# Kernel optimization log

Measured on AMD Instinct MI355X. Metric: run time of the kernel, lower is better.

Reference implementation:

```python
import jax, jax.numpy as jnp
import numpy as np

B, N, K, D, V, L = 16, 512, 16, 256, 64, 2


def setup_inputs() -> dict:
    key = jax.random.key(0)
    ks = jax.random.split(key, 20)
    inp = {
        "node_reps": jax.random.normal(ks[0], (B, N, D), dtype=jnp.float32),
        "mask": jax.random.uniform(ks[1], (B, N), dtype=jnp.float32),
        "in_indices": jax.random.randint(ks[2], (B, N, K), 0, N),
        "in_edges": jax.random.randint(ks[3], (B, N, K), 0, V),
        "in_mask": jax.random.uniform(ks[4], (B, N, K), dtype=jnp.float32),
        "out_indices": jax.random.randint(ks[5], (B, N, K), 0, N),
        "out_edges": jax.random.randint(ks[6], (B, N, K), 0, V),
        "out_mask": jax.random.uniform(ks[7], (B, N, K), dtype=jnp.float32),
        "edge_emb": jax.random.normal(ks[8], (V, D), dtype=jnp.float32) * 0.02,
        # packed gate weights, order [ig, fg, og, cell] along last dim
        "Wi": jax.random.normal(ks[9], (2 * D, 4 * D), dtype=jnp.float32) * 0.02,
        "Wo": jax.random.normal(ks[10], (2 * D, 4 * D), dtype=jnp.float32) * 0.02,
        "Ui": jax.random.normal(ks[11], (2 * D, 4 * D), dtype=jnp.float32) * 0.02,
        "Uo": jax.random.normal(ks[12], (2 * D, 4 * D), dtype=jnp.float32) * 0.02,
        "bi": jnp.zeros((4 * D,), dtype=jnp.float32),
        "bo": jnp.zeros((4 * D,), dtype=jnp.float32),
        "bui": jnp.zeros((4 * D,), dtype=jnp.float32),
        "buo": jnp.zeros((4 * D,), dtype=jnp.float32),
    }
    return inp


def _agg(h, idx, edge_reps, nmask):
    # gather neighbor states: [B,N,K,D]
    neigh = h[jnp.arange(h.shape[0])[:, None, None], idx]
    x = jnp.concatenate([neigh, edge_reps], axis=-1) * nmask[..., None]
    return x.sum(axis=2)  # [B,N,2D]


def reference(node_reps, mask, in_indices, in_edges, in_mask,
              out_indices, out_edges, out_mask,
              edge_emb, Wi, Wo, Ui, Uo, bi, bo, bui, buo):
    in_edge_reps = edge_emb[in_edges]    # [B,N,K,D]
    out_edge_reps = edge_emb[out_edges]  # [B,N,K,D]

    in_reps = _agg(node_reps, in_indices, in_edge_reps, in_mask)     # [B,N,2D]
    out_reps = _agg(node_reps, out_indices, out_edge_reps, out_mask)  # [B,N,2D]
    z_static = in_reps @ Wi + bi + out_reps @ Wo + bo  # [B,N,4D]

    h = node_reps
    c = jnp.zeros_like(node_reps)
    reps = []
    for _ in range(L):
        in_pre = _agg(h, in_indices, in_edge_reps, in_mask)
        out_pre = _agg(h, out_indices, out_edge_reps, out_mask)
        z = z_static + in_pre @ Ui + bui + out_pre @ Uo + buo  # [B,N,4D]
        ig, fg, og, ci = jnp.split(z, 4, axis=-1)
        ig = jax.nn.sigmoid(ig)
        fg = jax.nn.sigmoid(fg)
        og = jax.nn.sigmoid(og)
        ci = jnp.tanh(ci)
        c_new = fg * c + ig * ci
        h_new = og * jnp.tanh(c_new)
        c = c_new * mask[..., None]
        h = h_new * mask[..., None]
        reps.append(h)
    return (jnp.stack(reps, axis=0), h, c)
```

## Files before the change

### kernel.cpp

```cpp
#include <hip/hip_runtime.h>
#include <math.h>

#define Kn 16
#define Dd 256
#define NC 1024
#define MR 8192

typedef _Float16 h8 __attribute__((ext_vector_type(8)));
typedef _Float16 h4 __attribute__((ext_vector_type(4)));
typedef _Float16 h2 __attribute__((ext_vector_type(2)));
typedef float f4 __attribute__((ext_vector_type(4)));

__device__ __forceinline__ void gload16(_Float16* lds, const _Float16* g) {
  __builtin_amdgcn_global_load_lds(
      (const __attribute__((address_space(1))) void*)g,
      (__attribute__((address_space(3))) void*)lds, 16, 0, 0);
}

__device__ __forceinline__ float fsigm(float x) { return 1.f / (1.f + __expf(-x)); }
__device__ __forceinline__ float ftanh(float x) { return 2.f / (1.f + __expf(-2.f * x)) - 1.f; }

__global__ __launch_bounds__(256) void prep_kernel(
    const float* __restrict__ node_reps, const float* __restrict__ emb,
    const int* __restrict__ iidx, const float* __restrict__ im,
    const int* __restrict__ oidx, const float* __restrict__ om,
    const int* __restrict__ ie, const int* __restrict__ oe,
    const float* __restrict__ Wi, const float* __restrict__ Wo,
    const float* __restrict__ Ui, const float* __restrict__ Uo,
    const float* __restrict__ bi, const float* __restrict__ bo,
    const float* __restrict__ bui, const float* __restrict__ buo,
    _Float16* __restrict__ X, _Float16* __restrict__ W0f,
    _Float16* __restrict__ Wlf, float* __restrict__ biasq,
    _Float16* __restrict__ n16) {
  __shared__ __align__(16) char smem[40960];
  const int b = blockIdx.x, t = threadIdx.x;

  if (b < 64) {
    float* seT = (float*)smem;
    float* sa = (float*)(smem + 8192);
    const int vgrp = b >> 2, cq = b & 3;
    const int dir = vgrp >> 3;
    const int v0 = (vgrp & 7) * 8;
    const float* Wa = dir ? Wo : Wi;
    const float* Ua = dir ? Uo : Ui;
#pragma unroll
    for (int r = 0; r < 8; r++) seT[t * 8 + r] = emb[(v0 + r) * 256 + t];
    __syncthreads();

    const int l = t & 63, ds = t >> 6;
    const int cp0 = cq * 256 + l * 4;
    const int g = (cp0 >> 4) & 3;
    const int d0 = ((cp0 >> 6) << 4) + (cp0 & 15);
    const int c0 = g * 256 + d0;
    const float* wp = Wa + (size_t)(256 + ds * 64) * NC + c0;
    const float* up = Ua + (size_t)(256 + ds * 64) * NC + c0;
    const float* sT = seT + (ds * 64) * 8;

    f4 av[8] = {};
    for (int bb8 = 0; bb8 < 8; bb8++) {
      f4 wv8[8], uv8[8];
#pragma unroll
      for (int ii = 0; ii < 8; ii++) {
        const int dd = bb8 * 8 + ii;
        wv8[ii] = *(const f4*)(wp + (size_t)dd * NC);
        uv8[ii] = *(const f4*)(up + (size_t)dd * NC);
      }
      __builtin_amdgcn_sched_barrier(0);
#pragma unroll
      for (int ii = 0; ii < 8; ii++) {
        const int dd = bb8 * 8 + ii;
        const f4 wv = wv8[ii] + uv8[ii];
        const f4 s0 = *(const f4*)&sT[dd * 8];
        const f4 s1 = *(const f4*)&sT[dd * 8 + 4];
        av[0] += s0[0] * wv; av[1] += s0[1] * wv;
        av[2] += s0[2] * wv; av[3] += s0[3] * wv;
        av[4] += s1[0] * wv; av[5] += s1[1] * wv;
        av[6] += s1[2] * wv; av[7] += s1[3] * wv;
      }
    }
#pragma unroll
    for (int r = 0; r < 8; r++) *(f4*)&sa[((ds * 8 + r) * 64 + l) * 4] = av[r];
    __syncthreads();
#pragma unroll
    for (int it = 0; it < 2; it++) {
      const int item = t + it * 256;
      const int r = item >> 6, fl = item & 63;
      f4 s = {0.f, 0.f, 0.f, 0.f};
#pragma unroll
      for (int d = 0; d < 4; d++) s += *(const f4*)&sa[((d * 8 + r) * 64 + fl) * 4];
      const int vvg = vgrp * 8 + r;
      const int kt = 16 + (vvg >> 5);
      const int lhi = (vvg >> 3) & 3;
      const int j = vvg & 7;
      const int cpb = cq * 256 + fl * 4;
#pragma unroll
      for (int i = 0; i < 4; i++) {
        const int cp = cpb + i;
        W0f[kt * 32768 + (cp >> 4) * 512 + (lhi * 16 + (cp & 15)) * 8 + j] = (_Float16)s[i];
      }
    }
  } else if (b < 96) {
    const int p = b - 64;
    const int kk = t >> 3;
    const int tc = t & 7;
    const int k = (p & 15) * 32 + kk;
    const float* rowp;
    const float* rowp2 = nullptr;
    if (p < 16) {
      rowp  = (k < 256) ? Wi + (size_t)k * NC : Wo + (size_t)(k - 256) * NC;
      rowp2 = (k < 256) ? Ui + (size_t)k * NC : Uo + (size_t)(k - 256) * NC;
    } else {
      rowp  = (k < 256) ? Ui + (size_t)k * NC : Uo + (size_t)(k - 256) * NC;
    }
    _Float16* dst = (p < 16) ? (W0f + p * 32768) : (Wlf + (p - 16) * 32768);
    const int lane0 = (kk >> 3) * 16;
    const int j = kk & 7;
    for (int bb8 = 0; bb8 < 4; bb8++) {
      f4 w8[8], u8[8];
#pragma unroll
      for (int ii = 0; ii < 8; ii++) {
        const int c = (bb8 * 8 + ii) * 32 + tc * 4;
        w8[ii] = *(const f4*)(rowp + c);
        if (p < 16) u8[ii] = *(const f4*)(rowp2 + c);
      }
      __builtin_amdgcn_sched_barrier(0);
#pragma unroll
      for (int ii = 0; ii < 8; ii++) {
        const int c = (bb8 * 8 + ii) * 32 + tc * 4;
        const int g = c >> 8, d = c & 255;
        const int nt = 4 * (d >> 4) + g;
        const int lb = lane0 + (d & 15);
        f4 v = w8[ii];
        if (p < 16) v += u8[ii];
#pragma unroll
        for (int q = 0; q < 4; q++)
          dst[nt * 512 + (lb + q) * 8 + j] = (_Float16)v[q];
      }
    }
  } else if (b < 224) {
    const int cb = b - 96;
#pragma unroll
    for (int r = 0; r < 8; r++) {
      const int off = cb * 16384 + r * 2048 + t * 8;
      const f4 v0 = *(const f4*)(node_reps + off);
      const f4 v1 = *(const f4*)(node_reps + off + 4);
      h8 o;
#pragma unroll
      for (int jj = 0; jj < 4; jj++) { o[jj] = (_Float16)v0[jj]; o[jj + 4] = (_Float16)v1[jj]; }
      *(h8*)&n16[off] = o;
    }
  } else if (b < 736) {
    const int lane = t & 63;
    const int wid = t >> 6;
    const int half = lane >> 5;
    const int sel = lane >> 4, p16 = lane & 15;
    const int vmine = 2 * lane - half * 64;
#pragma unroll
    for (int j = 0; j < 4; j++) {
      const int row = (b - 224) * 16 + wid * 4 + j;
      const int bb = row * Kn + p16;
      const int* ap = (sel == 0)   ? (iidx + bb)
                      : (sel == 1) ? ((const int*)im + bb)
                      : (sel == 2) ? (oidx + bb)
                                   : ((const int*)om + bb);
      const int cmb = *ap;
      const int cmbe = *(((lane & 16) ? oe : ie) + bb);
      float b0 = 0.f, b1 = 0.f;
#pragma unroll
      for (int k = 0; k < 16; k++) {
        const int ec = __shfl(cmbe, (half << 4) | k, 64);
        const float mc = __int_as_float(__shfl(cmb, (lane & 32) | 16 | k, 64));
        b0 += (ec == vmine) ? mc : 0.f;
        b1 += (ec == vmine + 1) ? mc : 0.f;
      }
      h2 bp;
      bp[0] = (_Float16)b0;
      bp[1] = (_Float16)b1;
      *(h2*)&X[(size_t)row * NC + 512 + lane * 2] = bp;
    }
  } else {
#pragma unroll
    for (int i = 0; i < 4; i++) {
      const int cq = t * 4 + i;
      const int dd = cq >> 2, g = cq & 3;
      const int c = g * 256 + dd;
      biasq[cq] = bi[c] + bo[c] + bui[c] + buo[c];
    }
  }
}

__global__ __launch_bounds__(256, 4) void agg_kernel(
    const _Float16* __restrict__ src,
    const int* __restrict__ iidx, const float* __restrict__ im,
    const int* __restrict__ oidx, const float* __restrict__ om,
    _Float16* __restrict__ X) {
  const int lane = threadIdx.x & 63;
  const int wid = threadIdx.x >> 6;
  const int b = blockIdx.x;
  const int row = (b & 7) * 1024 + (b >> 3) * 4 + wid;
  const int half = lane >> 5;
  const int lc = lane & 31;
  const int sel = lane >> 4, p16 = lane & 15;

  const int bb = row * Kn + p16;
  const int* ap = (sel == 0)   ? (iidx + bb)
                  : (sel == 1) ? ((const int*)im + bb)
                  : (sel == 2) ? (oidx + bb)
                               : ((const int*)om + bb);
  const int cmb = *ap;

  const int hb = row & ~511;
  const _Float16* hp = src + ((size_t)hb << 8) + (lc << 3);

  h8 w[16];
#pragma unroll
  for (int k = 0; k < 16; k++) {
    const int ik = __shfl(cmb, (lane & 32) | k, 64);
    w[k] = *(const h8*)(hp + ((size_t)ik << 8));
  }
  __builtin_amdgcn_sched_barrier(0);

  float acc[8] = {};
#pragma unroll
  for (int k = 0; k < 16; k++) {
    const float mk = __int_as_float(__shfl(cmb, (lane & 32) | 16 | k, 64));
#pragma unroll
    for (int c = 0; c < 8; c++) acc[c] += mk * (float)w[k][c];
  }

  h8 o;
#pragma unroll
  for (int c = 0; c < 8; c++) o[c] = (_Float16)acc[c];
  *(h8*)&X[(size_t)row * NC + half * 256 + lc * 8] = o;
}

template <bool WITH_Z>
__global__ __launch_bounds__(256) void fused_gemm(
    const _Float16* __restrict__ A, const _Float16* __restrict__ Wf,
    const float* __restrict__ biasq, _Float16* __restrict__ zq,
    const float* __restrict__ mask, const float* __restrict__ node_reps,
    float* __restrict__ reps, float* __restrict__ hbuf,
    _Float16* __restrict__ d16, float* __restrict__ cbuf) {
  constexpr int KT = WITH_Z ? 20 : 16;
  constexpr int D = 4;
  __shared__ __align__(16) _Float16 lds[3][8192];

  const int wg = (blockIdx.x & 7) * 64 + (blockIdx.x >> 3);
  const int bm = wg >> 3, bn = wg & 7;
  const int tid = threadIdx.x, lane = tid & 63, wid = tid >> 6;
  const int wr = wid >> 1, wc = wid & 1;
  const int lr = lane & 15, lg = lane >> 4;

  f4 acc[4][4] = {};

  const _Float16* srcA0 = A + (size_t)(bm * 128 + 2 * wid * 16 + lr) * NC + lg * 8;
  const _Float16* srcB0 = Wf + ((size_t)bn * 8 + 2 * wid) * 512 + lane * 8;
  const int woff = 2 * wid * 512;

  auto stage = [&](int buf, int kt) {
    _Float16* base = lds[buf];
    const _Float16* sa = srcA0 + kt * 32;
    gload16(base + woff, sa);
    gload16(base + woff + 512, sa + 16 * NC);
    const _Float16* sb = srcB0 + (size_t)kt * 32768;
    gload16(base + 4096 + woff, sb);
    gload16(base + 4096 + woff + 512, sb + 512);
  };

  stage(0, 0);
  stage(1, 1);
  asm volatile("s_waitcnt vmcnt(%0)" :: "i"(D) : "memory");
  __builtin_amdgcn_s_barrier();

  int cur = 0;
  for (int kt = 0; kt < KT; kt++) {
    if (kt + 2 < KT) stage(cur == 0 ? 2 : cur - 1, kt + 2);

    const _Float16* base = lds[cur];
    h8 a[4], bfr[4];
#pragma unroll
    for (int m = 0; m < 4; m++) a[m] = *(const h8*)&base[(wr * 4 + m) * 512 + lane * 8];
#pragma unroll
    for (int n = 0; n < 4; n++) bfr[n] = *(const h8*)&base[4096 + (wc * 4 + n) * 512 + lane * 8];
    asm volatile("s_waitcnt lgkmcnt(0)" ::: "memory");
    __builtin_amdgcn_sched_barrier(0);

    __builtin_amdgcn_s_setprio(1);
#pragma unroll
    for (int m = 0; m < 4; m++)
#pragma unroll
      for (int n = 0; n < 4; n++)
        acc[m][n] = __builtin_amdgcn_mfma_f32_16x16x32_f16(a[m], bfr[n], acc[m][n], 0, 0, 0);
    __builtin_amdgcn_s_setprio(0);

    if (kt + 2 < KT) asm volatile("s_waitcnt vmcnt(%0)" :: "i"(D) : "memory");
    else             asm volatile("s_waitcnt vmcnt(0)" ::: "memory");
    __builtin_amdgcn_sched_barrier(0);
    __builtin_amdgcn_s_barrier();

    cur = (cur == 2) ? 0 : cur + 1;
  }

  const int d = (bn * 2 + wc) * 16 + lr;
  const int row0 = bm * 128 + wr * 64;
  f4 bq = {0.f, 0.f, 0.f, 0.f};
  if (WITH_Z) bq = *(const f4*)&biasq[d * 4];
#pragma unroll
  for (int i = 0; i < 4; i++) {
#pragma unroll
    for (int r = 0; r < 4; r++) {
      const int row = row0 + i * 16 + lg * 4 + r;
      const size_t off = (size_t)row * Dd + d;
      float zi, zf, zo, zc;
      if (WITH_Z) {
        zi = acc[i][0][r] + bq.x;
        zf = acc[i][1][r] + bq.y;
        zo = acc[i][2][r] + bq.z;
        zc = acc[i][3][r] + bq.w;
        h4 oz;
        oz[0] = (_Float16)zi; oz[1] = (_Float16)zf;
        oz[2] = (_Float16)zo; oz[3] = (_Float16)zc;
        *(h4*)&zq[off * 4] = oz;
      } else {
        const h4 zb = *(const h4*)&zq[off * 4];
        zi = (float)zb[0] + acc[i][0][r];
        zf = (float)zb[1] + acc[i][1][r];
        zo = (float)zb[2] + acc[i][2][r];
        zc = (float)zb[3] + acc[i][3][r];
      }
      const float ig = fsigm(zi), fg = fsigm(zf), og = fsigm(zo), ci = ftanh(zc);
      const float cold = WITH_Z ? 0.f : cbuf[off];
      const float cn = fg * cold + ig * ci;
      const float hn = og * ftanh(cn);
      const float mk = mask[row];
      cbuf[off] = cn * mk;
      const float hm = hn * mk;
      reps[off] = hm;
      if (WITH_Z) d16[off] = (_Float16)(hm - node_reps[off]);
      else        hbuf[off] = hm;
    }
  }
}

extern "C" void kernel_launch(void* const* d_in, const int* in_sizes, int n_in,
                              void* d_out, int out_size, void* d_ws, size_t ws_size,
                              hipStream_t stream) {
  const float* node_reps = (const float*)d_in[0];
  const float* mask      = (const float*)d_in[1];
  const int*   in_idx    = (const int*)d_in[2];
  const int*   in_edges  = (const int*)d_in[3];
  const float* in_mask   = (const float*)d_in[4];
  const int*   out_idx   = (const int*)d_in[5];
  const int*   out_edges = (const int*)d_in[6];
  const float* out_mask  = (const float*)d_in[7];
  const float* edge_emb  = (const float*)d_in[8];
  const float* Wi  = (const float*)d_in[9];
  const float* Wo  = (const float*)d_in[10];
  const float* Ui  = (const float*)d_in[11];
  const float* Uo  = (const float*)d_in[12];
  const float* bi  = (const float*)d_in[13];
  const float* bo  = (const float*)d_in[14];
  const float* bui = (const float*)d_in[15];
  const float* buo = (const float*)d_in[16];

  float* out = (float*)d_out;
  const size_t MD = (size_t)MR * Dd;
  float* reps0 = out;
  float* reps1 = out + MD;
  float* hbuf  = out + 2 * MD;
  float* cbuf  = out + 3 * MD;

  _Float16* X    = (_Float16*)d_ws;
  _Float16* zq   = X + (size_t)MR * NC;
  _Float16* W0f  = zq + (size_t)MR * NC;
  _Float16* Wlf  = W0f + 640 * 1024;
  _Float16* n16  = Wlf + 512 * 1024;
  _Float16* d16  = n16 + (size_t)MR * Dd;
  float*    biasq = (float*)(d16 + (size_t)MR * Dd);

  prep_kernel<<<737, 256, 0, stream>>>(node_reps, edge_emb, in_idx, in_mask,
                                       out_idx, out_mask, in_edges, out_edges,
                                       Wi, Wo, Ui, Uo, bi, bo, bui, buo,
                                       X, W0f, Wlf, biasq, n16);
  agg_kernel<<<2048, 256, 0, stream>>>(n16, in_idx, in_mask, out_idx, out_mask, X);
  fused_gemm<true><<<512, 256, 0, stream>>>(
      X, W0f, biasq, zq, mask, node_reps, reps0, nullptr, d16, cbuf);
  agg_kernel<<<2048, 256, 0, stream>>>(d16, in_idx, in_mask, out_idx, out_mask, X);
  fused_gemm<false><<<512, 256, 0, stream>>>(
      X, Wlf, nullptr, zq, mask, nullptr, reps1, hbuf, nullptr, cbuf);
}
```

Baseline: 78.05 us.

## Fuse prep and first aggregation into one kernel, gathering fp32 node reps directly

Merges the prep kernel and the first agg_kernel launch into a single kernel. The first neighbor aggregation now gathers fp32 node_reps directly instead of reading an fp16 copy, so the n16 conversion pass and one launch go away. Edge-count blocks are folded into the aggregation rows, and the edge-embedding projection work is split across more, smaller blocks (4 vocab rows per block instead of 8). The trade-off is that the fp32 gathers move twice the bytes per neighbor, and the small weight-prep blocks now share a launch with the large aggregation grid.

```diff
diff --git a/kernel.cpp b/kernel.cpp
--- a/kernel.cpp
+++ b/kernel.cpp
@@ -20,7 +20,7 @@
 __device__ __forceinline__ float fsigm(float x) { return 1.f / (1.f + __expf(-x)); }
 __device__ __forceinline__ float ftanh(float x) { return 2.f / (1.f + __expf(-2.f * x)) - 1.f; }
 
-__global__ __launch_bounds__(256) void prep_kernel(
+__global__ __launch_bounds__(256, 4) void mega2_kernel(
     const float* __restrict__ node_reps, const float* __restrict__ emb,
     const int* __restrict__ iidx, const float* __restrict__ im,
     const int* __restrict__ oidx, const float* __restrict__ om,
@@ -30,21 +30,83 @@
     const float* __restrict__ bi, const float* __restrict__ bo,
     const float* __restrict__ bui, const float* __restrict__ buo,
     _Float16* __restrict__ X, _Float16* __restrict__ W0f,
-    _Float16* __restrict__ Wlf, float* __restrict__ biasq,
-    _Float16* __restrict__ n16) {
-  __shared__ __align__(16) char smem[40960];
+    _Float16* __restrict__ Wlf, float* __restrict__ biasq) {
+  __shared__ __align__(16) char smem[20480];
   const int b = blockIdx.x, t = threadIdx.x;
 
-  if (b < 64) {
+  if (b < 2048) {
+    const int lane = t & 63;
+    const int wid = t >> 6;
+    const int row = (b & 7) * 1024 + (b >> 3) * 4 + wid;
+    const int half = lane >> 5;
+    const int lc = lane & 31;
+    const int sel = lane >> 4, p16 = lane & 15;
+
+    const int bb = row * Kn + p16;
+    const int* ap = (sel == 0)   ? (iidx + bb)
+                    : (sel == 1) ? ((const int*)im + bb)
+                    : (sel == 2) ? (oidx + bb)
+                                 : ((const int*)om + bb);
+    const int cmb = *ap;
+    const int cmbe = *(((lane & 16) ? oe : ie) + bb);
+
+    const int hb = row & ~511;
+    const float* hp = node_reps + ((size_t)hb << 8) + (lc << 3);
+
+    float acc[8] = {};
+#pragma unroll
+    for (int kb = 0; kb < 2; kb++) {
+      f4 w0[8], w1[8];
+#pragma unroll
+      for (int k = 0; k < 8; k++) {
+        const int ik = __shfl(cmb, (lane & 32) | (kb * 8 + k), 64);
+        const float* p = hp + ((size_t)ik << 8);
+        w0[k] = *(const f4*)p;
+        w1[k] = *(const f4*)(p + 4);
+      }
+      __builtin_amdgcn_sched_barrier(0);
+#pragma unroll
+      for (int k = 0; k < 8; k++) {
+        const float mk = __int_as_float(__shfl(cmb, (lane & 32) | 16 | (kb * 8 + k), 64));
+#pragma unroll
+        for (int c = 0; c < 4; c++) {
+          acc[c] += mk * w0[k][c];
+          acc[4 + c] += mk * w1[k][c];
+        }
+      }
+    }
+
+    {
+      float b0 = 0.f, b1 = 0.f;
+      const int vmine = 2 * lane - half * 64;
+#pragma unroll
+      for (int k = 0; k < 16; k++) {
+        const int ec = __shfl(cmbe, (half << 4) | k, 64);
+        const float mc = __int_as_float(__shfl(cmb, (lane & 32) | 16 | k, 64));
+        b0 += (ec == vmine) ? mc : 0.f;
+        b1 += (ec == vmine + 1) ? mc : 0.f;
+      }
+      h2 bp;
+      bp[0] = (_Float16)b0;
+      bp[1] = (_Float16)b1;
+      *(h2*)&X[(size_t)row * NC + 512 + lane * 2] = bp;
+    }
+
+    h8 o;
+#pragma unroll
+    for (int c = 0; c < 8; c++) o[c] = (_Float16)acc[c];
+    *(h8*)&X[(size_t)row * NC + half * 256 + lc * 8] = o;
+  } else if (b < 2176) {
     float* seT = (float*)smem;
-    float* sa = (float*)(smem + 8192);
-    const int vgrp = b >> 2, cq = b & 3;
-    const int dir = vgrp >> 3;
-    const int v0 = (vgrp & 7) * 8;
+    float* sa = (float*)(smem + 4096);
+    const int pb = b - 2048;
+    const int vgrp = pb >> 2, cq = pb & 3;
+    const int dir = vgrp >> 4;
+    const int v0 = (vgrp & 15) * 4;
     const float* Wa = dir ? Wo : Wi;
     const float* Ua = dir ? Uo : Ui;
 #pragma unroll
-    for (int r = 0; r < 8; r++) seT[t * 8 + r] = emb[(v0 + r) * 256 + t];
+    for (int r = 0; r < 4; r++) seT[t * 4 + r] = emb[(v0 + r) * 256 + t];
     __syncthreads();
 
     const int l = t & 63, ds = t >> 6;
@@ -54,9 +116,9 @@
     const int c0 = g * 256 + d0;
     const float* wp = Wa + (size_t)(256 + ds * 64) * NC + c0;
     const float* up = Ua + (size_t)(256 + ds * 64) * NC + c0;
-    const float* sT = seT + (ds * 64) * 8;
-
-    f4 av[8] = {};
+    const float* sT = seT + (ds * 64) * 4;
+
+    f4 av[4] = {};
     for (int bb8 = 0; bb8 < 8; bb8++) {
       f4 wv8[8], uv8[8];
 #pragma unroll
@@ -70,25 +132,22 @@
       for (int ii = 0; ii < 8; ii++) {
         const int dd = bb8 * 8 + ii;
         const f4 wv = wv8[ii] + uv8[ii];
-        const f4 s0 = *(const f4*)&sT[dd * 8];
-        const f4 s1 = *(const f4*)&sT[dd * 8 + 4];
-        av[0] += s0[0] * wv; av[1] += s0[1] * wv;
-        av[2] += s0[2] * wv; av[3] += s0[3] * wv;
-        av[4] += s1[0] * wv; av[5] += s1[1] * wv;
-        av[6] += s1[2] * wv; av[7] += s1[3] * wv;
-      }
-    }
-#pragma unroll
-    for (int r = 0; r < 8; r++) *(f4*)&sa[((ds * 8 + r) * 64 + l) * 4] = av[r];
+        const f4 s0 = *(const f4*)&sT[dd * 4];
+        av[0] += s0[0] * wv;
+        av[1] += s0[1] * wv;
+        av[2] += s0[2] * wv;
+        av[3] += s0[3] * wv;
+      }
+    }
+#pragma unroll
+    for (int r = 0; r < 4; r++) *(f4*)&sa[((ds * 4 + r) * 64 + l) * 4] = av[r];
     __syncthreads();
-#pragma unroll
-    for (int it = 0; it < 2; it++) {
-      const int item = t + it * 256;
-      const int r = item >> 6, fl = item & 63;
+    {
+      const int r = t >> 6, fl = t & 63;
       f4 s = {0.f, 0.f, 0.f, 0.f};
 #pragma unroll
-      for (int d = 0; d < 4; d++) s += *(const f4*)&sa[((d * 8 + r) * 64 + fl) * 4];
-      const int vvg = vgrp * 8 + r;
+      for (int d = 0; d < 4; d++) s += *(const f4*)&sa[((d * 4 + r) * 64 + fl) * 4];
+      const int vvg = vgrp * 4 + r;
       const int kt = 16 + (vvg >> 5);
       const int lhi = (vvg >> 3) & 3;
       const int j = vvg & 7;
@@ -99,8 +158,8 @@
         W0f[kt * 32768 + (cp >> 4) * 512 + (lhi * 16 + (cp & 15)) * 8 + j] = (_Float16)s[i];
       }
     }
-  } else if (b < 96) {
-    const int p = b - 64;
+  } else if (b < 2208) {
+    const int p = b - 2176;
     const int kk = t >> 3;
     const int tc = t & 7;
     const int k = (p & 15) * 32 + kk;
@@ -136,47 +195,6 @@
         for (int q = 0; q < 4; q++)
           dst[nt * 512 + (lb + q) * 8 + j] = (_Float16)v[q];
       }
-    }
-  } else if (b < 224) {
-    const int cb = b - 96;
-#pragma unroll
-    for (int r = 0; r < 8; r++) {
-      const int off = cb * 16384 + r * 2048 + t * 8;
-      const f4 v0 = *(const f4*)(node_reps + off);
-      const f4 v1 = *(const f4*)(node_reps + off + 4);
-      h8 o;
-#pragma unroll
-      for (int jj = 0; jj < 4; jj++) { o[jj] = (_Float16)v0[jj]; o[jj + 4] = (_Float16)v1[jj]; }
-      *(h8*)&n16[off] = o;
-    }
-  } else if (b < 736) {
-    const int lane = t & 63;
-    const int wid = t >> 6;
-    const int half = lane >> 5;
-    const int sel = lane >> 4, p16 = lane & 15;
-    const int vmine = 2 * lane - half * 64;
-#pragma unroll
-    for (int j = 0; j < 4; j++) {
-      const int row = (b - 224) * 16 + wid * 4 + j;
-      const int bb = row * Kn + p16;
-      const int* ap = (sel == 0)   ? (iidx + bb)
-                      : (sel == 1) ? ((const int*)im + bb)
-                      : (sel == 2) ? (oidx + bb)
-                                   : ((const int*)om + bb);
-      const int cmb = *ap;
-      const int cmbe = *(((lane & 16) ? oe : ie) + bb);
-      float b0 = 0.f, b1 = 0.f;
-#pragma unroll
-      for (int k = 0; k < 16; k++) {
-        const int ec = __shfl(cmbe, (half << 4) | k, 64);
-        const float mc = __int_as_float(__shfl(cmb, (lane & 32) | 16 | k, 64));
-        b0 += (ec == vmine) ? mc : 0.f;
-        b1 += (ec == vmine + 1) ? mc : 0.f;
-      }
-      h2 bp;
-      bp[0] = (_Float16)b0;
-      bp[1] = (_Float16)b1;
-      *(h2*)&X[(size_t)row * NC + 512 + lane * 2] = bp;
     }
   } else {
 #pragma unroll
@@ -374,15 +392,13 @@
   _Float16* zq   = X + (size_t)MR * NC;
   _Float16* W0f  = zq + (size_t)MR * NC;
   _Float16* Wlf  = W0f + 640 * 1024;
-  _Float16* n16  = Wlf + 512 * 1024;
-  _Float16* d16  = n16 + (size_t)MR * Dd;
+  _Float16* d16  = Wlf + 512 * 1024;
   float*    biasq = (float*)(d16 + (size_t)MR * Dd);
 
-  prep_kernel<<<737, 256, 0, stream>>>(node_reps, edge_emb, in_idx, in_mask,
-                                       out_idx, out_mask, in_edges, out_edges,
-                                       Wi, Wo, Ui, Uo, bi, bo, bui, buo,
-                                       X, W0f, Wlf, biasq, n16);
-  agg_kernel<<<2048, 256, 0, stream>>>(n16, in_idx, in_mask, out_idx, out_mask, X);
+  mega2_kernel<<<2209, 256, 0, stream>>>(node_reps, edge_emb, in_idx, in_mask,
+                                         out_idx, out_mask, in_edges, out_edges,
+                                         Wi, Wo, Ui, Uo, bi, bo, bui, buo,
+                                         X, W0f, Wlf, biasq);
   fused_gemm<true><<<512, 256, 0, stream>>>(
       X, W0f, biasq, zq, mask, node_reps, reps0, nullptr, d16, cbuf);
   agg_kernel<<<2048, 256, 0, stream>>>(d16, in_idx, in_mask, out_idx, out_mask, X);
```

Result: no change. 76.87 us (-1.5%).
